# Performance work log

Hardware: AMD Instinct MI355X
Metric: run time of the kernel (lower is better)

The kernel has to match this reference:

```python
import jax, jax.numpy as jnp
import numpy as np

D = 6  # hardcoded feature dim from nn.Linear(6, 6)
NEG = -1000000.0


def setup_inputs() -> dict:
    key = jax.random.key(0)
    ks = jax.random.split(key, 8)
    B, S = 32, 2048
    X = jax.random.normal(ks[0], (B, S, D), dtype=jnp.float32)
    attention_mask = jax.random.randint(ks[1], (B, S), 0, 2).astype(jnp.int32)
    # torch nn.Linear params: weight [out,in], bias [out]
    lim = 1.0 / np.sqrt(D)
    Wq = jax.random.uniform(ks[2], (D, D), jnp.float32, -lim, lim)
    bq = jax.random.uniform(ks[3], (D,), jnp.float32, -lim, lim)
    Wk = jax.random.uniform(ks[4], (D, D), jnp.float32, -lim, lim)
    bk = jax.random.uniform(ks[5], (D,), jnp.float32, -lim, lim)
    Wv = jax.random.uniform(ks[6], (D, D), jnp.float32, -lim, lim)
    bv = jax.random.uniform(ks[7], (D,), jnp.float32, -lim, lim)
    return {"X": X, "attention_mask": attention_mask,
            "Wq": Wq, "bq": bq, "Wk": Wk, "bk": bk, "Wv": Wv, "bv": bv}


def reference(X, attention_mask, Wq, bq, Wk, bk, Wv, bv):
    # Linear projections (torch Linear: x @ W^T + b)
    Q = X @ Wq.T + bq  # [B,S,D]
    K = X @ Wk.T + bk
    V = X @ Wv.T + bv
    score = jnp.einsum('bsd,btd->bst', Q, K)  # [B,S,S]
    m1 = (attention_mask == 0)[:, :, None]  # mask rows
    m2 = (attention_mask == 0)[:, None, :]  # mask cols
    score = jnp.where(m1 | m2, NEG, score)
    weight = jax.nn.softmax(score, axis=-1)
    return jnp.einsum('bst,btd->bsd', weight, V)
```

## Files before the change

kernel.cpp:

```cpp
#include <hip/hip_runtime.h>

#define SEQ 2048
#define DIM 6
#define NSEG 8
#define SEGR (SEQ / NSEG)
#define VROW 2056

typedef _Float16 half4F __attribute__((ext_vector_type(4)));
typedef short bf16x4 __attribute__((ext_vector_type(4)));
typedef float f32x4 __attribute__((ext_vector_type(4)));

union FragU { uint2 u; half4F h; bf16x4 b; };

__device__ __forceinline__ unsigned pkh(float a, float b) {
    return __builtin_bit_cast(unsigned, __builtin_amdgcn_cvt_pkrtz(a, b));
}
__device__ __forceinline__ unsigned bf16rn(float x) {
    unsigned u = __builtin_bit_cast(unsigned, x);
    return (u + 0x7FFFu + ((u >> 16) & 1u)) >> 16;
}
__device__ __forceinline__ unsigned pkbf(float a, float b) {
    return bf16rn(a) | (bf16rn(b) << 16);
}
__device__ __forceinline__ unsigned pkbf_trunc(float a, float b) {
    return __builtin_amdgcn_perm(__builtin_bit_cast(unsigned, b),
                                 __builtin_bit_cast(unsigned, a),
                                 0x07060302u);
}

__device__ __forceinline__ f32x4 mfma_bf16_(bf16x4 a, bf16x4 b, f32x4 c) {
#if __has_builtin(__builtin_amdgcn_mfma_f32_16x16x16bf16_1k)
    return __builtin_amdgcn_mfma_f32_16x16x16bf16_1k(a, b, c, 0, 0, 0);
#else
    f32x4 d;
    asm("v_mfma_f32_16x16x16_bf16 %0, %1, %2, %3"
        : "=v"(d) : "v"(a), "v"(b), "v"(c));
    return d;
#endif
}


__launch_bounds__(256)
__global__ void prep(const float* __restrict__ X, const int* __restrict__ mask,
                     const float* __restrict__ Wk, const float* __restrict__ bk,
                     const float* __restrict__ Wv, const float* __restrict__ bv,
                     __fp16* __restrict__ Kc, unsigned short* __restrict__ Vc,
                     unsigned short* __restrict__ rowl,
                     float* __restrict__ vsumP, int* __restrict__ nuArr) {
    __shared__ unsigned char msk[SEQ];
    __shared__ int sA[256], sB[256];
    __shared__ float vred[4][8];
    const int b = blockIdx.x >> 3, seg = blockIdx.x & 7;
    const int tid = threadIdx.x;
    const int* mb = mask + (size_t)b * SEQ;
    const float L2E = 1.44269504088896f;

    int cnt = 0;
#pragma unroll
    for (int j = 0; j < 8; ++j) {
        const int m = (mb[tid * 8 + j] != 0);
        msk[tid * 8 + j] = (unsigned char)m;
        cnt += m;
    }
    sA[tid] = cnt;
    __syncthreads();
    int* src = sA; int* dst = sB;
    for (int off = 1; off < 256; off <<= 1) {
        int v = src[tid];
        if (tid >= off) v += src[tid - off];
        dst[tid] = v;
        __syncthreads();
        int* tmp = src; src = dst; dst = tmp;
    }
    if (seg == 0 && tid == 0) nuArr[b] = src[255];

    const int t = seg * SEGR + tid;
    const int i8 = t >> 3;
    int slot = (i8 > 0) ? src[i8 - 1] : 0;
    for (int j = i8 * 8; j < t; ++j) slot += msk[j];

    const float2* xp = reinterpret_cast<const float2*>(X + ((size_t)b * SEQ + t) * DIM);
    float2 x01 = xp[0], x23 = xp[1], x45 = xp[2];
    float x[DIM] = {x01.x, x01.y, x23.x, x23.y, x45.x, x45.y};
    float kk[DIM], vv[DIM];
#pragma unroll
    for (int r = 0; r < DIM; ++r) {
        float k = bk[r], v = bv[r];
#pragma unroll
        for (int c = 0; c < DIM; ++c) {
            k = fmaf(Wk[r * DIM + c], x[c], k);
            v = fmaf(Wv[r * DIM + c], x[c], v);
        }
        kk[r] = k * L2E;
        vv[r] = v;
    }
    if (msk[t]) {
        uint4 kw;
        kw.x = pkh(kk[0], kk[1]);
        kw.y = pkh(kk[2], kk[3]);
        kw.z = pkh(kk[4], kk[5]);
        kw.w = 0u;
        *reinterpret_cast<uint4*>(Kc + ((size_t)b * SEQ + slot) * 8) = kw;
        uint4 vw;
        vw.x = pkbf(vv[0], vv[1]);
        vw.y = pkbf(vv[2], vv[3]);
        vw.z = pkbf(vv[4], vv[5]);
        vw.w = 0u;
        *reinterpret_cast<uint4*>(Vc + ((size_t)b * SEQ + slot) * 8) = vw;
        rowl[(size_t)b * SEQ + slot] = (unsigned short)t;
    }

    const int lane = tid & 63, wid = tid >> 6;
#pragma unroll
    for (int r = 0; r < DIM; ++r) {
        float s = vv[r];
#pragma unroll
        for (int off = 1; off < 64; off <<= 1) s += __shfl_xor(s, off);
        if (lane == 0) vred[wid][r] = s;
    }
    __syncthreads();
    if (tid < DIM) {
        vsumP[((size_t)b * NSEG + seg) * 8 + tid] =
            vred[0][tid] + vred[1][tid] + vred[2][tid] + vred[3][tid];
    }
}

__launch_bounds__(512, 2)
__global__ void attn_mfma(const float* __restrict__ X,
                          const int* __restrict__ mask,
                          const float* __restrict__ Wq, const float* __restrict__ bq,
                          const __fp16* __restrict__ Kc,
                          const unsigned short* __restrict__ Vc,
                          const unsigned short* __restrict__ rowl,
                          const float* __restrict__ vsumP,
                          const int* __restrict__ nuArr,
                          float* __restrict__ out) {
    __shared__ __align__(16) __fp16 Ksm[SEQ * 8];
    __shared__ __align__(16) unsigned short Vt[7 * VROW];

    const int b = blockIdx.x >> 4, blk = blockIdx.x & 15;
    const int tid = threadIdx.x;
    const int Nu = nuArr[b];

    if (tid < 128) {
        const int t = blk * 128 + tid;
        if (mask[(size_t)b * SEQ + t] == 0) {
            float* o = out + ((size_t)b * SEQ + t) * DIM;
#pragma unroll
            for (int r = 0; r < DIM; ++r) {
                float s = 0.0f;
#pragma unroll
                for (int g2 = 0; g2 < NSEG; ++g2)
                    s += vsumP[((size_t)b * NSEG + g2) * 8 + r];
                o[r] = s * (1.0f / SEQ);
            }
        }
    }

    const int rowbase = blk * 128;
    if (rowbase >= Nu) return;
    const int NT16 = (Nu + 15) & ~15;

    const uint4* kg = reinterpret_cast<const uint4*>(Kc + (size_t)b * SEQ * 8);
    const uint4* vg = reinterpret_cast<const uint4*>(Vc + (size_t)b * SEQ * 8);
    for (int i = tid; i < NT16; i += 512) {
        uint4 kw, vw;
        if (i < Nu) { kw = kg[i]; vw = vg[i]; }
        else { kw = make_uint4(0, 0, 0, pkh(-1024.0f, 0.0f)); vw = make_uint4(0, 0, 0, 0); }
        reinterpret_cast<uint4*>(Ksm)[i] = kw;
        Vt[0 * VROW + i] = (unsigned short)(vw.x & 0xFFFFu);
        Vt[1 * VROW + i] = (unsigned short)(vw.x >> 16);
        Vt[2 * VROW + i] = (unsigned short)(vw.y & 0xFFFFu);
        Vt[3 * VROW + i] = (unsigned short)(vw.y >> 16);
        Vt[4 * VROW + i] = (unsigned short)(vw.z & 0xFFFFu);
        Vt[5 * VROW + i] = (unsigned short)(vw.z >> 16);
        Vt[6 * VROW + i] = (i < Nu) ? 0x3F80u : 0u;
    }
    __syncthreads();

    const int lane = tid & 63, wid = tid >> 6;
    const int s0 = rowbase + wid * 16;
    if (s0 >= Nu) return;
    const int r15 = lane & 15, g = lane >> 4;
    const int sidx = s0 + r15;
    const int srow = rowl[(size_t)b * SEQ + (sidx < Nu ? sidx : Nu - 1)];

    float qq[DIM];
    {
        const float2* xp =
            reinterpret_cast<const float2*>(X + ((size_t)b * SEQ + srow) * DIM);
        float2 x01 = xp[0], x23 = xp[1], x45 = xp[2];
        float x[DIM] = {x01.x, x01.y, x23.x, x23.y, x45.x, x45.y};
#pragma unroll
        for (int r = 0; r < DIM; ++r) {
            float q = bq[r];
#pragma unroll
            for (int c = 0; c < DIM; ++c) q = fmaf(Wq[r * DIM + c], x[c], q);
            qq[r] = q;
        }
    }
    FragU qf;
    qf.u.x = (g == 0) ? pkh(qq[0], qq[1]) : (g == 1) ? pkh(qq[4], qq[5]) : 0u;
    qf.u.y = (g == 0) ? pkh(qq[2], qq[3]) : (g == 1) ? pkh(1.0f, 0.0f) : 0u;

    const f32x4 zero4 = {0.0f, 0.0f, 0.0f, 0.0f};
    f32x4 acc = zero4;
    {
        const int dcl = (r15 < 6) ? r15 : 6;
        int kidx = r15 * 8 + (g & 1) * 4;
        int vidx = dcl * VROW + g * 4;
        const int ntiles = NT16 >> 4;
#pragma unroll 4
        for (int tt = 0; tt < ntiles; ++tt) {
            half4F kf = *reinterpret_cast<const half4F*>(&Ksm[kidx]);
            bf16x4 vf = *reinterpret_cast<const bf16x4*>(&Vt[vidx]);
            f32x4 d = __builtin_amdgcn_mfma_f32_16x16x16f16(kf, qf.h, zero4, 0, 0, 0);
            FragU pa;
            pa.u.x = pkbf_trunc(__builtin_amdgcn_exp2f(d[0]),
                                __builtin_amdgcn_exp2f(d[1]));
            pa.u.y = pkbf_trunc(__builtin_amdgcn_exp2f(d[2]),
                                __builtin_amdgcn_exp2f(d[3]));
            acc = mfma_bf16_(pa.b, vf, acc);
            kidx += 128;
            vidx += 16;
        }
    }

    const int srcl = (lane & 48) | 6;
#pragma unroll
    for (int r = 0; r < 4; ++r) {
        const float dnm = __shfl(acc[r], srcl);
        const float val = acc[r] * __builtin_amdgcn_rcpf(dnm);
        const int oidx = s0 + g * 4 + r;
        if (r15 < 6 && oidx < Nu) {
            const int orow = rowl[(size_t)b * SEQ + oidx];
            out[((size_t)b * SEQ + orow) * DIM + r15] = val;
        }
    }
}

extern "C" void kernel_launch(void* const* d_in, const int* in_sizes, int n_in,
                              void* d_out, int out_size, void* d_ws, size_t ws_size,
                              hipStream_t stream) {
    const float* X  = (const float*)d_in[0];
    const int* mask = (const int*)d_in[1];
    const float* Wq = (const float*)d_in[2];
    const float* bq = (const float*)d_in[3];
    const float* Wk = (const float*)d_in[4];
    const float* bk = (const float*)d_in[5];
    const float* Wv = (const float*)d_in[6];
    const float* bv = (const float*)d_in[7];
    float* out = (float*)d_out;

    const int B = in_sizes[0] / (SEQ * DIM);

    __fp16* Kc = (__fp16*)d_ws;
    unsigned short* Vc = (unsigned short*)(Kc + (size_t)B * SEQ * 8);
    unsigned short* rowl = Vc + (size_t)B * SEQ * 8;
    float* vsumP = (float*)(rowl + (size_t)B * SEQ);
    int* nuArr = (int*)(vsumP + (size_t)B * NSEG * 8);

    prep<<<dim3(B * NSEG), 256, 0, stream>>>(X, mask, Wk, bk, Wv, bv,
                                             Kc, Vc, rowl, vsumP, nuArr);
    attn_mfma<<<dim3(B * 16), 512, 0, stream>>>(X, mask, Wq, bq, Kc, Vc, rowl,
                                                vsumP, nuArr, out);
}
```

Measured before the change: 24.01 us.

## Split key loop across wave pairs and use wave-shuffle scan in prep

The attention kernel now assigns each 16-row query tile to a pair of waves that split the key tiles between them and combine partial accumulators through shared memory. Query tiles are interleaved across all 16 blocks of a batch, so work is balanced whether the unmasked count is small or large, instead of only the early blocks doing work. The prep kernel's multi-barrier shared-memory scan is replaced by a wave-level shuffle scan plus a four-entry cross-wave total. This adds a shared-memory combine and extra barriers per pass, moves to dynamic shared memory, and calls hipFuncSetAttribute on every launch.

```diff
diff --git a/kernel.cpp b/kernel.cpp
--- a/kernel.cpp
+++ b/kernel.cpp
@@ -48,10 +48,12 @@
                      unsigned short* __restrict__ rowl,
                      float* __restrict__ vsumP, int* __restrict__ nuArr) {
     __shared__ unsigned char msk[SEQ];
-    __shared__ int sA[256], sB[256];
+    __shared__ int wexcl[256];
+    __shared__ int wtot[4];
     __shared__ float vred[4][8];
     const int b = blockIdx.x >> 3, seg = blockIdx.x & 7;
     const int tid = threadIdx.x;
+    const int lane = tid & 63, wid = tid >> 6;
     const int* mb = mask + (size_t)b * SEQ;
     const float L2E = 1.44269504088896f;
 
@@ -62,21 +64,27 @@
         msk[tid * 8 + j] = (unsigned char)m;
         cnt += m;
     }
-    sA[tid] = cnt;
+    int inc = cnt;
+#pragma unroll
+    for (int off = 1; off < 64; off <<= 1) {
+        const int t2 = __shfl_up(inc, off);
+        if (lane >= off) inc += t2;
+    }
+    wexcl[tid] = inc - cnt;
+    if (lane == 63) wtot[wid] = inc;
     __syncthreads();
-    int* src = sA; int* dst = sB;
-    for (int off = 1; off < 256; off <<= 1) {
-        int v = src[tid];
-        if (tid >= off) v += src[tid - off];
-        dst[tid] = v;
-        __syncthreads();
-        int* tmp = src; src = dst; dst = tmp;
-    }
-    if (seg == 0 && tid == 0) nuArr[b] = src[255];
+    const int Nu = wtot[0] + wtot[1] + wtot[2] + wtot[3];
+    if (seg == 0 && tid == 0) nuArr[b] = Nu;
 
     const int t = seg * SEGR + tid;
     const int i8 = t >> 3;
-    int slot = (i8 > 0) ? src[i8 - 1] : 0;
+    int slot = wexcl[i8];
+    {
+        const int w = i8 >> 6;
+        if (w > 0) slot += wtot[0];
+        if (w > 1) slot += wtot[1];
+        if (w > 2) slot += wtot[2];
+    }
     for (int j = i8 * 8; j < t; ++j) slot += msk[j];
 
     const float2* xp = reinterpret_cast<const float2*>(X + ((size_t)b * SEQ + t) * DIM);
@@ -110,7 +118,6 @@
         rowl[(size_t)b * SEQ + slot] = (unsigned short)t;
     }
 
-    const int lane = tid & 63, wid = tid >> 6;
 #pragma unroll
     for (int r = 0; r < DIM; ++r) {
         float s = vv[r];
@@ -135,12 +142,18 @@
                           const float* __restrict__ vsumP,
                           const int* __restrict__ nuArr,
                           float* __restrict__ out) {
-    __shared__ __align__(16) __fp16 Ksm[SEQ * 8];
-    __shared__ __align__(16) unsigned short Vt[7 * VROW];
+    extern __shared__ __align__(16) char smem[];
+    __fp16* Ksm = (__fp16*)smem;
+    unsigned short* Vt = (unsigned short*)(smem + 32768);
+    f32x4* comb = (f32x4*)(smem + 32768 + 7 * VROW * 2);
 
     const int b = blockIdx.x >> 4, blk = blockIdx.x & 15;
     const int tid = threadIdx.x;
     const int Nu = nuArr[b];
+    const int NT16 = (Nu + 15) & ~15;
+    const int ntiles = NT16 >> 4;
+    const int nstile = (Nu + 15) >> 4;
+    const int npass = (nstile + 63) >> 6;
 
     if (tid < 128) {
         const int t = blk * 128 + tid;
@@ -156,10 +169,6 @@
             }
         }
     }
-
-    const int rowbase = blk * 128;
-    if (rowbase >= Nu) return;
-    const int NT16 = (Nu + 15) & ~15;
 
     const uint4* kg = reinterpret_cast<const uint4*>(Kc + (size_t)b * SEQ * 8);
     const uint4* vg = reinterpret_cast<const uint4*>(Vc + (size_t)b * SEQ * 8);
@@ -179,63 +188,74 @@
     __syncthreads();
 
     const int lane = tid & 63, wid = tid >> 6;
-    const int s0 = rowbase + wid * 16;
-    if (s0 >= Nu) return;
+    const int pair = wid >> 1, half = wid & 1;
     const int r15 = lane & 15, g = lane >> 4;
-    const int sidx = s0 + r15;
-    const int srow = rowl[(size_t)b * SEQ + (sidx < Nu ? sidx : Nu - 1)];
-
-    float qq[DIM];
-    {
-        const float2* xp =
-            reinterpret_cast<const float2*>(X + ((size_t)b * SEQ + srow) * DIM);
-        float2 x01 = xp[0], x23 = xp[1], x45 = xp[2];
-        float x[DIM] = {x01.x, x01.y, x23.x, x23.y, x45.x, x45.y};
-#pragma unroll
-        for (int r = 0; r < DIM; ++r) {
-            float q = bq[r];
-#pragma unroll
-            for (int c = 0; c < DIM; ++c) q = fmaf(Wq[r * DIM + c], x[c], q);
-            qq[r] = q;
-        }
-    }
-    FragU qf;
-    qf.u.x = (g == 0) ? pkh(qq[0], qq[1]) : (g == 1) ? pkh(qq[4], qq[5]) : 0u;
-    qf.u.y = (g == 0) ? pkh(qq[2], qq[3]) : (g == 1) ? pkh(1.0f, 0.0f) : 0u;
-
+    const int dcl = (r15 < 6) ? r15 : 6;
     const f32x4 zero4 = {0.0f, 0.0f, 0.0f, 0.0f};
-    f32x4 acc = zero4;
-    {
-        const int dcl = (r15 < 6) ? r15 : 6;
-        int kidx = r15 * 8 + (g & 1) * 4;
-        int vidx = dcl * VROW + g * 4;
-        const int ntiles = NT16 >> 4;
-#pragma unroll 4
-        for (int tt = 0; tt < ntiles; ++tt) {
-            half4F kf = *reinterpret_cast<const half4F*>(&Ksm[kidx]);
-            bf16x4 vf = *reinterpret_cast<const bf16x4*>(&Vt[vidx]);
-            f32x4 d = __builtin_amdgcn_mfma_f32_16x16x16f16(kf, qf.h, zero4, 0, 0, 0);
-            FragU pa;
-            pa.u.x = pkbf_trunc(__builtin_amdgcn_exp2f(d[0]),
-                                __builtin_amdgcn_exp2f(d[1]));
-            pa.u.y = pkbf_trunc(__builtin_amdgcn_exp2f(d[2]),
-                                __builtin_amdgcn_exp2f(d[3]));
-            acc = mfma_bf16_(pa.b, vf, acc);
-            kidx += 128;
-            vidx += 16;
-        }
-    }
-
-    const int srcl = (lane & 48) | 6;
-#pragma unroll
-    for (int r = 0; r < 4; ++r) {
-        const float dnm = __shfl(acc[r], srcl);
-        const float val = acc[r] * __builtin_amdgcn_rcpf(dnm);
-        const int oidx = s0 + g * 4 + r;
-        if (r15 < 6 && oidx < Nu) {
-            const int orow = rowl[(size_t)b * SEQ + oidx];
-            out[((size_t)b * SEQ + orow) * DIM + r15] = val;
-        }
+
+    for (int pass = 0; pass < npass; ++pass) {
+        const int rt = pass * 64 + blk * 4 + pair;
+        const bool active = (rt < nstile);
+        f32x4 acc = zero4;
+        if (active) {
+            const int s0 = rt * 16;
+            const int sidx = s0 + r15;
+            const int srow = rowl[(size_t)b * SEQ + (sidx < Nu ? sidx : Nu - 1)];
+            float qq[DIM];
+            {
+                const float2* xp = reinterpret_cast<const float2*>(
+                    X + ((size_t)b * SEQ + srow) * DIM);
+                float2 x01 = xp[0], x23 = xp[1], x45 = xp[2];
+                float x[DIM] = {x01.x, x01.y, x23.x, x23.y, x45.x, x45.y};
+#pragma unroll
+                for (int r = 0; r < DIM; ++r) {
+                    float q = bq[r];
+#pragma unroll
+                    for (int c = 0; c < DIM; ++c)
+                        q = fmaf(Wq[r * DIM + c], x[c], q);
+                    qq[r] = q;
+                }
+            }
+            FragU qf;
+            qf.u.x = (g == 0) ? pkh(qq[0], qq[1]) : (g == 1) ? pkh(qq[4], qq[5]) : 0u;
+            qf.u.y = (g == 0) ? pkh(qq[2], qq[3]) : (g == 1) ? pkh(1.0f, 0.0f) : 0u;
+
+            int kidx = half * 128 + r15 * 8 + (g & 1) * 4;
+            int vidx = dcl * VROW + half * 16 + g * 4;
+#pragma unroll 2
+            for (int tt = half; tt < ntiles; tt += 2) {
+                half4F kf = *reinterpret_cast<const half4F*>(&Ksm[kidx]);
+                bf16x4 vf = *reinterpret_cast<const bf16x4*>(&Vt[vidx]);
+                f32x4 d = __builtin_amdgcn_mfma_f32_16x16x16f16(kf, qf.h, zero4, 0, 0, 0);
+                FragU pa;
+                pa.u.x = pkbf_trunc(__builtin_amdgcn_exp2f(d[0]),
+                                    __builtin_amdgcn_exp2f(d[1]));
+                pa.u.y = pkbf_trunc(__builtin_amdgcn_exp2f(d[2]),
+                                    __builtin_amdgcn_exp2f(d[3]));
+                acc = mfma_bf16_(pa.b, vf, acc);
+                kidx += 256;
+                vidx += 32;
+            }
+        }
+        if (half == 1 && active) comb[pair * 64 + lane] = acc;
+        __syncthreads();
+        if (half == 0 && active) {
+            const f32x4 oth = comb[pair * 64 + lane];
+            acc = acc + oth;
+            const int s0 = rt * 16;
+            const int srcl = (lane & 48) | 6;
+#pragma unroll
+            for (int r = 0; r < 4; ++r) {
+                const float dnm = __shfl(acc[r], srcl);
+                const float val = acc[r] * __builtin_amdgcn_rcpf(dnm);
+                const int oidx = s0 + g * 4 + r;
+                if (r15 < 6 && oidx < Nu) {
+                    const int orow = rowl[(size_t)b * SEQ + oidx];
+                    out[((size_t)b * SEQ + orow) * DIM + r15] = val;
+                }
+            }
+        }
+        __syncthreads();
     }
 }
 
@@ -260,8 +280,12 @@
     float* vsumP = (float*)(rowl + (size_t)B * SEQ);
     int* nuArr = (int*)(vsumP + (size_t)B * NSEG * 8);
 
+    const size_t shmem = 32768 + (size_t)7 * VROW * 2 + 4096;
+    hipFuncSetAttribute(reinterpret_cast<const void*>(attn_mfma),
+                        hipFuncAttributeMaxDynamicSharedMemorySize, (int)shmem);
+
     prep<<<dim3(B * NSEG), 256, 0, stream>>>(X, mask, Wk, bk, Wv, bv,
                                              Kc, Vc, rowl, vsumP, nuArr);
-    attn_mfma<<<dim3(B * 16), 512, 0, stream>>>(X, mask, Wq, bq, Kc, Vc, rowl,
-                                                vsumP, nuArr, out);
-}
+    attn_mfma<<<dim3(B * 16), 512, shmem, stream>>>(X, mask, Wq, bq, Kc, Vc, rowl,
+                                                    vsumP, nuArr, out);
+}
```

Result: no change. 23.85 us (-0.6%).

## Batch LDS loads into 8-tile chunks and use wave-shuffle prefix scan

Applied to the files above, without the earlier changes.

The attention inner loop now processes key tiles in chunks of 8, loading all K and V fragments from LDS before issuing the MFMA/exp chain. This overlaps LDS latency with compute, and the padded key count is rounded up to 128 so the chunks divide evenly, which adds some masked padding work. The prep kernel's block-wide Hillis-Steele scan, which needed a barrier per step, is replaced by a wave-level shuffle scan plus per-wave totals, cutting the barriers to one.

```diff
diff --git a/kernel.cpp b/kernel.cpp
--- a/kernel.cpp
+++ b/kernel.cpp
@@ -5,6 +5,7 @@
 #define NSEG 8
 #define SEGR (SEQ / NSEG)
 #define VROW 2056
+#define CH 8
 
 typedef _Float16 half4F __attribute__((ext_vector_type(4)));
 typedef short bf16x4 __attribute__((ext_vector_type(4)));
@@ -48,10 +49,12 @@
                      unsigned short* __restrict__ rowl,
                      float* __restrict__ vsumP, int* __restrict__ nuArr) {
     __shared__ unsigned char msk[SEQ];
-    __shared__ int sA[256], sB[256];
+    __shared__ int wexcl[256];
+    __shared__ int wtot[4];
     __shared__ float vred[4][8];
     const int b = blockIdx.x >> 3, seg = blockIdx.x & 7;
     const int tid = threadIdx.x;
+    const int lane = tid & 63, wid = tid >> 6;
     const int* mb = mask + (size_t)b * SEQ;
     const float L2E = 1.44269504088896f;
 
@@ -62,21 +65,27 @@
         msk[tid * 8 + j] = (unsigned char)m;
         cnt += m;
     }
-    sA[tid] = cnt;
+    int inc = cnt;
+#pragma unroll
+    for (int off = 1; off < 64; off <<= 1) {
+        const int t2 = __shfl_up(inc, off);
+        if (lane >= off) inc += t2;
+    }
+    wexcl[tid] = inc - cnt;
+    if (lane == 63) wtot[wid] = inc;
     __syncthreads();
-    int* src = sA; int* dst = sB;
-    for (int off = 1; off < 256; off <<= 1) {
-        int v = src[tid];
-        if (tid >= off) v += src[tid - off];
-        dst[tid] = v;
-        __syncthreads();
-        int* tmp = src; src = dst; dst = tmp;
-    }
-    if (seg == 0 && tid == 0) nuArr[b] = src[255];
+    const int Nu = wtot[0] + wtot[1] + wtot[2] + wtot[3];
+    if (seg == 0 && tid == 0) nuArr[b] = Nu;
 
     const int t = seg * SEGR + tid;
     const int i8 = t >> 3;
-    int slot = (i8 > 0) ? src[i8 - 1] : 0;
+    int slot = wexcl[i8];
+    {
+        const int w = i8 >> 6;
+        if (w > 0) slot += wtot[0];
+        if (w > 1) slot += wtot[1];
+        if (w > 2) slot += wtot[2];
+    }
     for (int j = i8 * 8; j < t; ++j) slot += msk[j];
 
     const float2* xp = reinterpret_cast<const float2*>(X + ((size_t)b * SEQ + t) * DIM);
@@ -110,7 +119,6 @@
         rowl[(size_t)b * SEQ + slot] = (unsigned short)t;
     }
 
-    const int lane = tid & 63, wid = tid >> 6;
 #pragma unroll
     for (int r = 0; r < DIM; ++r) {
         float s = vv[r];
@@ -141,6 +149,7 @@
     const int b = blockIdx.x >> 4, blk = blockIdx.x & 15;
     const int tid = threadIdx.x;
     const int Nu = nuArr[b];
+    const int NTC = (Nu + CH * 16 - 1) & ~(CH * 16 - 1);
 
     if (tid < 128) {
         const int t = blk * 128 + tid;
@@ -159,11 +168,10 @@
 
     const int rowbase = blk * 128;
     if (rowbase >= Nu) return;
-    const int NT16 = (Nu + 15) & ~15;
 
     const uint4* kg = reinterpret_cast<const uint4*>(Kc + (size_t)b * SEQ * 8);
     const uint4* vg = reinterpret_cast<const uint4*>(Vc + (size_t)b * SEQ * 8);
-    for (int i = tid; i < NT16; i += 512) {
+    for (int i = tid; i < NTC; i += 512) {
         uint4 kw, vw;
         if (i < Nu) { kw = kg[i]; vw = vg[i]; }
         else { kw = make_uint4(0, 0, 0, pkh(-1024.0f, 0.0f)); vw = make_uint4(0, 0, 0, 0); }
@@ -209,20 +217,27 @@
         const int dcl = (r15 < 6) ? r15 : 6;
         int kidx = r15 * 8 + (g & 1) * 4;
         int vidx = dcl * VROW + g * 4;
-        const int ntiles = NT16 >> 4;
-#pragma unroll 4
-        for (int tt = 0; tt < ntiles; ++tt) {
-            half4F kf = *reinterpret_cast<const half4F*>(&Ksm[kidx]);
-            bf16x4 vf = *reinterpret_cast<const bf16x4*>(&Vt[vidx]);
-            f32x4 d = __builtin_amdgcn_mfma_f32_16x16x16f16(kf, qf.h, zero4, 0, 0, 0);
-            FragU pa;
-            pa.u.x = pkbf_trunc(__builtin_amdgcn_exp2f(d[0]),
-                                __builtin_amdgcn_exp2f(d[1]));
-            pa.u.y = pkbf_trunc(__builtin_amdgcn_exp2f(d[2]),
-                                __builtin_amdgcn_exp2f(d[3]));
-            acc = mfma_bf16_(pa.b, vf, acc);
-            kidx += 128;
-            vidx += 16;
+        const int nchunk = NTC >> (4 + 3);
+        for (int c = 0; c < nchunk; ++c) {
+            half4F kf[CH];
+            bf16x4 vf[CH];
+#pragma unroll
+            for (int u = 0; u < CH; ++u) {
+                kf[u] = *reinterpret_cast<const half4F*>(&Ksm[kidx + u * 128]);
+                vf[u] = *reinterpret_cast<const bf16x4*>(&Vt[vidx + u * 16]);
+            }
+#pragma unroll
+            for (int u = 0; u < CH; ++u) {
+                f32x4 d = __builtin_amdgcn_mfma_f32_16x16x16f16(kf[u], qf.h, zero4, 0, 0, 0);
+                FragU pa;
+                pa.u.x = pkbf_trunc(__builtin_amdgcn_exp2f(d[0]),
+                                    __builtin_amdgcn_exp2f(d[1]));
+                pa.u.y = pkbf_trunc(__builtin_amdgcn_exp2f(d[2]),
+                                    __builtin_amdgcn_exp2f(d[3]));
+                acc = mfma_bf16_(pa.b, vf[u], acc);
+            }
+            kidx += CH * 128;
+            vidx += CH * 16;
         }
     }
 
```

Measured after the change: 22.77 us. -5.2%, faster.
